# Kernel optimization log

Hardware: AMD Instinct MI355X
Metric: run time of the kernel (lower is better)

Reference implementation:

```python
import jax, jax.numpy as jnp
import numpy as np
from jax import lax

B, S, H, NH, E, L, V = 8, 512, 512, 8, 8, 6, 32000
DH = H // NH
FF = 4 * H
EPS_LN = 1e-5
EPS_GATE = 1e-8


def setup_inputs() -> dict:
    key = jax.random.key(0)
    ks = jax.random.split(key, 20)
    s = 0.02
    f = jnp.float32
    return {
        'input_ids': jax.random.randint(ks[0], (B, S), 0, V),
        'emb': (jax.random.normal(ks[1], (V, H)) * s).astype(f),
        'pos_emb': (jax.random.normal(ks[2], (S, H)) * s).astype(f),
        'attn_in_w': (jax.random.normal(ks[3], (L, 3 * H, H)) * s).astype(f),
        'attn_in_b': jnp.zeros((L, 3 * H), f),
        'attn_out_w': (jax.random.normal(ks[4], (L, H, H)) * s).astype(f),
        'attn_out_b': jnp.zeros((L, H), f),
        'ln1_g': jnp.ones((L, H), f),
        'ln1_b': jnp.zeros((L, H), f),
        'gate_w': (jax.random.normal(ks[5], (L, E, H)) * s).astype(f),
        'w1': (jax.random.normal(ks[6], (L, E, FF, H)) * s).astype(f),
        'b1': jnp.zeros((L, E, FF), f),
        'w2': (jax.random.normal(ks[7], (L, E, H, FF)) * s).astype(f),
        'b2': jnp.zeros((L, E, H), f),
        'ln2_g': jnp.ones((L, H), f),
        'ln2_b': jnp.zeros((L, H), f),
        'lnf_g': jnp.ones((H,), f),
        'lnf_b': jnp.zeros((H,), f),
        'lm_w': (jax.random.normal(ks[8], (V, H)) * s).astype(f),
    }


def _ln(x, g, b):
    m = jnp.mean(x, axis=-1, keepdims=True)
    v = jnp.mean(jnp.square(x - m), axis=-1, keepdims=True)
    return (x - m) * lax.rsqrt(v + EPS_LN) * g + b


def _forward(input_ids, emb, pos_emb, attn_in_w, attn_in_b, attn_out_w, attn_out_b,
             ln1_g, ln1_b, gate_w, w1, b1, w2, b2, ln2_g, ln2_b, lnf_g, lnf_b, lm_w):
    b_, s_ = input_ids.shape
    x = emb[input_ids] + pos_emb[jnp.arange(s_)][None]  # [B,S,H]

    def layer(x, p):
        in_w, in_b, out_w, out_b, l1g, l1b, gw, W1, B1, W2, B2, l2g, l2b = p
        # --- multi-head self attention (torch nn.MultiheadAttention math) ---
        qkv = x @ in_w.T + in_b                       # [B,S,3H]
        q, k, v = jnp.split(qkv, 3, axis=-1)
        q = q.reshape(b_, s_, NH, DH)
        k = k.reshape(b_, s_, NH, DH)
        v = v.reshape(b_, s_, NH, DH)
        scores = jnp.einsum('bqhd,bkhd->bhqk', q, k) / jnp.sqrt(jnp.float32(DH))
        att = jax.nn.softmax(scores, axis=-1)
        o = jnp.einsum('bhqk,bkhd->bqhd', att, v).reshape(b_, s_, H)
        o = o @ out_w.T + out_b
        x = _ln(x + o, l1g, l1b)
        # --- MoE MLP (top-1 switch routing) ---
        xf = x.reshape(-1, H)                          # [T,H]
        gate_scores = jax.nn.softmax(xf @ gw.T, axis=-1)  # [T,E]
        idx = jnp.argmax(gate_scores, axis=-1)         # [T]
        top = jnp.max(gate_scores, axis=-1)            # [T]
        gate = top / (top + EPS_GATE)                  # top-1 normalization
        hid = jax.nn.relu(jnp.einsum('th,efh->tef', xf, W1) + B1)  # [T,E,FF]
        ye = jnp.einsum('tef,ehf->teh', hid, W2) + B2               # [T,E,H]
        comb = jax.nn.one_hot(idx, E, dtype=xf.dtype) * gate[:, None]
        moe = jnp.einsum('te,teh->th', comb, ye)
        x = _ln(x + moe.reshape(b_, s_, H), l2g, l2b)
        # load balancing loss
        rp = gate_scores.mean(axis=0)
        eu = jax.nn.one_hot(idx, E, dtype=xf.dtype).mean(axis=0)
        lb = jnp.float32(E) * jnp.sum(rp * eu)
        return x, lb

    x, lbs = lax.scan(layer, x, (attn_in_w, attn_in_b, attn_out_w, attn_out_b,
                                 ln1_g, ln1_b, gate_w, w1, b1, w2, b2, ln2_g, ln2_b))
    logits = _ln(x, lnf_g, lnf_b) @ lm_w.T
    return logits, jnp.mean(lbs)


def reference(input_ids, emb, pos_emb, attn_in_w, attn_in_b, attn_out_w, attn_out_b,
              ln1_g, ln1_b, gate_w, w1, b1, w2, b2, ln2_g, ln2_b, lnf_g, lnf_b, lm_w):
    return _forward(input_ids, emb, pos_emb, attn_in_w, attn_in_b, attn_out_w, attn_out_b,
                    ln1_g, ln1_b, gate_w, w1, b1, w2, b2, ln2_g, ln2_b, lnf_g, lnf_b, lm_w)
```

## Files before the change

kernel.cpp:

```cpp
#include <hip/hip_runtime.h>
#include <math.h>


constexpr int CB = 8;
constexpr int CS = 512;
constexpr int CH = 512;
constexpr int CNH = 8;
constexpr int CDH = 64;
constexpr int CE = 8;
constexpr int CFF = 2048;
constexpr int CL = 6;
constexpr int CV = 32000;
constexpr int CT = CB * CS;
constexpr int CH3 = 3 * CH;

__global__ __launch_bounds__(64) void k_init(int* cnt, float* lbacc) {
  int tid = threadIdx.x;
  if (tid < CE) cnt[tid] = 0;
  if (tid == 0) *lbacc = 0.f;
}

__global__ __launch_bounds__(256) void k_embed(const int* __restrict__ ids,
                                               const float* __restrict__ emb,
                                               const float* __restrict__ pos,
                                               float* __restrict__ x) {
  int i = blockIdx.x * 256 + threadIdx.x;
  int t = i / (CH / 4);
  int h4 = i % (CH / 4);
  int id = ids[t];
  float4 e = ((const float4*)(emb + (size_t)id * CH))[h4];
  float4 p = ((const float4*)(pos + (size_t)(t % CS) * CH))[h4];
  float4 r;
  r.x = e.x + p.x; r.y = e.y + p.y; r.z = e.z + p.z; r.w = e.w + p.w;
  ((float4*)(x + (size_t)t * CH))[h4] = r;
}

__global__ __launch_bounds__(256) void k_gemm_bt(const float* __restrict__ A,
                                                 const float* __restrict__ W,
                                                 const float* __restrict__ bias,
                                                 float* __restrict__ C,
                                                 int N, int K) {
  __shared__ __align__(16) float As[16][64];
  __shared__ __align__(16) float Ws[16][64];
  int tid = threadIdx.x;
  int m0 = blockIdx.y * 64, n0 = blockIdx.x * 64;
  int lr = tid >> 2, lk = (tid & 3) << 2;
  int tx = tid & 15, ty = tid >> 4;
  float acc[4][4] = {};
  for (int k0 = 0; k0 < K; k0 += 16) {
    float4 a = *(const float4*)(A + (size_t)(m0 + lr) * K + k0 + lk);
    float4 w = *(const float4*)(W + (size_t)(n0 + lr) * K + k0 + lk);
    As[lk + 0][lr] = a.x; As[lk + 1][lr] = a.y; As[lk + 2][lr] = a.z; As[lk + 3][lr] = a.w;
    Ws[lk + 0][lr] = w.x; Ws[lk + 1][lr] = w.y; Ws[lk + 2][lr] = w.z; Ws[lk + 3][lr] = w.w;
    __syncthreads();
#pragma unroll
    for (int kk = 0; kk < 16; ++kk) {
      float ar[4], wr[4];
#pragma unroll
      for (int i = 0; i < 4; i++) ar[i] = As[kk][ty * 4 + i];
#pragma unroll
      for (int j = 0; j < 4; j++) wr[j] = Ws[kk][tx * 4 + j];
#pragma unroll
      for (int i = 0; i < 4; i++)
#pragma unroll
        for (int j = 0; j < 4; j++) acc[i][j] += ar[i] * wr[j];
    }
    __syncthreads();
  }
  float4 bv = make_float4(0.f, 0.f, 0.f, 0.f);
  if (bias) bv = *(const float4*)(bias + n0 + tx * 4);
#pragma unroll
  for (int i = 0; i < 4; i++) {
    float4 r;
    r.x = acc[i][0] + bv.x; r.y = acc[i][1] + bv.y;
    r.z = acc[i][2] + bv.z; r.w = acc[i][3] + bv.w;
    *(float4*)(C + (size_t)(m0 + ty * 4 + i) * N + n0 + tx * 4) = r;
  }
}

__global__ __launch_bounds__(256) void k_gemm_qk(const float* __restrict__ qkv,
                                                 float* __restrict__ sc) {
  int bh = blockIdx.z, b = bh >> 3, hd = bh & 7;
  const float* Qb = qkv + (size_t)b * CS * CH3 + hd * CDH;
  const float* Kb = Qb + CH;
  __shared__ __align__(16) float As[16][64];
  __shared__ __align__(16) float Bs[16][64];
  int tid = threadIdx.x;
  int m0 = blockIdx.y * 64, n0 = blockIdx.x * 64;
  int lr = tid >> 2, lk = (tid & 3) << 2;
  int tx = tid & 15, ty = tid >> 4;
  float acc[4][4] = {};
  for (int k0 = 0; k0 < CDH; k0 += 16) {
    float4 a = *(const float4*)(Qb + (size_t)(m0 + lr) * CH3 + k0 + lk);
    float4 w = *(const float4*)(Kb + (size_t)(n0 + lr) * CH3 + k0 + lk);
    As[lk + 0][lr] = a.x; As[lk + 1][lr] = a.y; As[lk + 2][lr] = a.z; As[lk + 3][lr] = a.w;
    Bs[lk + 0][lr] = w.x; Bs[lk + 1][lr] = w.y; Bs[lk + 2][lr] = w.z; Bs[lk + 3][lr] = w.w;
    __syncthreads();
#pragma unroll
    for (int kk = 0; kk < 16; ++kk) {
      float ar[4], wr[4];
#pragma unroll
      for (int i = 0; i < 4; i++) ar[i] = As[kk][ty * 4 + i];
#pragma unroll
      for (int j = 0; j < 4; j++) wr[j] = Bs[kk][tx * 4 + j];
#pragma unroll
      for (int i = 0; i < 4; i++)
#pragma unroll
        for (int j = 0; j < 4; j++) acc[i][j] += ar[i] * wr[j];
    }
    __syncthreads();
  }
#pragma unroll
  for (int i = 0; i < 4; i++) {
    float4 r;
    r.x = acc[i][0] * 0.125f; r.y = acc[i][1] * 0.125f;
    r.z = acc[i][2] * 0.125f; r.w = acc[i][3] * 0.125f;
    *(float4*)(sc + ((size_t)bh * CS + m0 + ty * 4 + i) * CS + n0 + tx * 4) = r;
  }
}

__global__ __launch_bounds__(256) void k_softmax(float* __restrict__ sc) {
  size_t row = blockIdx.x;
  float* r = sc + row * CS;
  int tid = threadIdx.x;
  float v0 = r[tid], v1 = r[tid + 256];
  __shared__ float red[4];
  __shared__ float bval;
  int lane = tid & 63, wid = tid >> 6;
  float m = fmaxf(v0, v1);
#pragma unroll
  for (int o = 32; o; o >>= 1) m = fmaxf(m, __shfl_down(m, o, 64));
  if (!lane) red[wid] = m;
  __syncthreads();
  if (!tid) bval = fmaxf(fmaxf(red[0], red[1]), fmaxf(red[2], red[3]));
  __syncthreads();
  float mx = bval;
  float e0 = expf(v0 - mx), e1 = expf(v1 - mx);
  float s = e0 + e1;
#pragma unroll
  for (int o = 32; o; o >>= 1) s += __shfl_down(s, o, 64);
  __syncthreads();
  if (!lane) red[wid] = s;
  __syncthreads();
  if (!tid) bval = red[0] + red[1] + red[2] + red[3];
  __syncthreads();
  float sum = bval;
  r[tid] = e0 / sum;
  r[tid + 256] = e1 / sum;
}

__global__ __launch_bounds__(256) void k_gemm_pv(const float* __restrict__ sc,
                                                 const float* __restrict__ qkv,
                                                 float* __restrict__ o) {
  int bh = blockIdx.z, b = bh >> 3, hd = bh & 7;
  const float* A = sc + (size_t)bh * CS * CS;
  const float* Vb = qkv + (size_t)b * CS * CH3 + 2 * CH + hd * CDH;
  __shared__ __align__(16) float As[16][64];
  __shared__ __align__(16) float Bs[16][64];
  int tid = threadIdx.x;
  int m0 = blockIdx.y * 64;
  int lr = tid >> 2, lk = (tid & 3) << 2;
  int jr = tid >> 4, dc = (tid & 15) << 2;
  int tx = tid & 15, ty = tid >> 4;
  float acc[4][4] = {};
  for (int k0 = 0; k0 < CS; k0 += 16) {
    float4 a = *(const float4*)(A + (size_t)(m0 + lr) * CS + k0 + lk);
    As[lk + 0][lr] = a.x; As[lk + 1][lr] = a.y; As[lk + 2][lr] = a.z; As[lk + 3][lr] = a.w;
    float4 v = *(const float4*)(Vb + (size_t)(k0 + jr) * CH3 + dc);
    *(float4*)&Bs[jr][dc] = v;
    __syncthreads();
#pragma unroll
    for (int kk = 0; kk < 16; ++kk) {
      float ar[4], br[4];
#pragma unroll
      for (int i = 0; i < 4; i++) ar[i] = As[kk][ty * 4 + i];
#pragma unroll
      for (int j = 0; j < 4; j++) br[j] = Bs[kk][tx * 4 + j];
#pragma unroll
      for (int i = 0; i < 4; i++)
#pragma unroll
        for (int j = 0; j < 4; j++) acc[i][j] += ar[i] * br[j];
    }
    __syncthreads();
  }
#pragma unroll
  for (int i = 0; i < 4; i++) {
    float4 r;
    r.x = acc[i][0]; r.y = acc[i][1]; r.z = acc[i][2]; r.w = acc[i][3];
    *(float4*)(o + ((size_t)b * CS + m0 + ty * 4 + i) * CH + hd * CDH + tx * 4) = r;
  }
}

__global__ __launch_bounds__(256) void k_add_ln(const float* __restrict__ xin,
                                                const float* __restrict__ resid,
                                                const float* __restrict__ g,
                                                const float* __restrict__ b,
                                                float* __restrict__ xout) {
  int t = blockIdx.x, tid = threadIdx.x;
  float v0 = xin[(size_t)t * CH + tid];
  float v1 = xin[(size_t)t * CH + tid + 256];
  if (resid) {
    v0 += resid[(size_t)t * CH + tid];
    v1 += resid[(size_t)t * CH + tid + 256];
  }
  __shared__ float red[4];
  __shared__ float stat;
  int lane = tid & 63, wid = tid >> 6;
  float s = v0 + v1;
#pragma unroll
  for (int o = 32; o; o >>= 1) s += __shfl_down(s, o, 64);
  if (!lane) red[wid] = s;
  __syncthreads();
  if (!tid) stat = (red[0] + red[1] + red[2] + red[3]) * (1.f / CH);
  __syncthreads();
  float m = stat;
  float d0 = v0 - m, d1 = v1 - m;
  float q = d0 * d0 + d1 * d1;
#pragma unroll
  for (int o = 32; o; o >>= 1) q += __shfl_down(q, o, 64);
  __syncthreads();
  if (!lane) red[wid] = q;
  __syncthreads();
  if (!tid) stat = rsqrtf((red[0] + red[1] + red[2] + red[3]) * (1.f / CH) + 1e-5f);
  __syncthreads();
  float rs = stat;
  xout[(size_t)t * CH + tid] = d0 * rs * g[tid] + b[tid];
  xout[(size_t)t * CH + tid + 256] = d1 * rs * g[tid + 256] + b[tid + 256];
}

__global__ __launch_bounds__(256) void k_gate(const float* __restrict__ xf,
                                              const float* __restrict__ gw,
                                              float* __restrict__ probs,
                                              float* __restrict__ gate,
                                              int* __restrict__ cnt,
                                              int* __restrict__ toklist) {
  int t = blockIdx.x, tid = threadIdx.x;
  float part[CE];
#pragma unroll
  for (int e = 0; e < CE; e++) part[e] = 0.f;
  for (int h = tid; h < CH; h += 256) {
    float xv = xf[(size_t)t * CH + h];
#pragma unroll
    for (int e = 0; e < CE; e++) part[e] += xv * gw[e * CH + h];
  }
  __shared__ float red[CE][4];
  int lane = tid & 63, wid = tid >> 6;
#pragma unroll
  for (int e = 0; e < CE; e++) {
    float v = part[e];
#pragma unroll
    for (int o = 32; o; o >>= 1) v += __shfl_down(v, o, 64);
    if (!lane) red[e][wid] = v;
  }
  __syncthreads();
  if (tid == 0) {
    float lg[CE], mx = -1e30f;
#pragma unroll
    for (int e = 0; e < CE; e++) {
      lg[e] = red[e][0] + red[e][1] + red[e][2] + red[e][3];
      mx = fmaxf(mx, lg[e]);
    }
    float p[CE], sum = 0.f;
#pragma unroll
    for (int e = 0; e < CE; e++) { p[e] = expf(lg[e] - mx); sum += p[e]; }
    float best = -1.f; int bi = 0;
#pragma unroll
    for (int e = 0; e < CE; e++) {
      p[e] /= sum;
      probs[(size_t)t * CE + e] = p[e];
      if (p[e] > best) { best = p[e]; bi = e; }
    }
    gate[t] = best / (best + 1e-8f);
    int pos = atomicAdd(&cnt[bi], 1);
    toklist[bi * CT + pos] = t;
  }
}

__global__ __launch_bounds__(256) void k_moe1(const float* __restrict__ xf,
                                              const float* __restrict__ w1,
                                              const float* __restrict__ b1,
                                              const int* __restrict__ cnt,
                                              const int* __restrict__ toklist,
                                              float* __restrict__ hid, int l) {
  int e = blockIdx.z;
  int n = cnt[e];
  int r0 = blockIdx.y * 64;
  if (r0 >= n) return;
  __shared__ int toks[64];
  int tid = threadIdx.x;
  if (tid < 64) toks[tid] = (r0 + tid < n) ? toklist[e * CT + r0 + tid] : -1;
  __syncthreads();
  const float* W = w1 + (size_t)(l * CE + e) * CFF * CH;
  const float* bb = b1 + (size_t)(l * CE + e) * CFF;
  int f0 = blockIdx.x * 64;
  __shared__ __align__(16) float As[16][64];
  __shared__ __align__(16) float Ws[16][64];
  int lr = tid >> 2, lk = (tid & 3) << 2;
  int tx = tid & 15, ty = tid >> 4;
  int tokA = toks[lr];
  float acc[4][4] = {};
  for (int k0 = 0; k0 < CH; k0 += 16) {
    float4 a = make_float4(0.f, 0.f, 0.f, 0.f);
    if (tokA >= 0) a = *(const float4*)(xf + (size_t)tokA * CH + k0 + lk);
    float4 w = *(const float4*)(W + (size_t)(f0 + lr) * CH + k0 + lk);
    As[lk + 0][lr] = a.x; As[lk + 1][lr] = a.y; As[lk + 2][lr] = a.z; As[lk + 3][lr] = a.w;
    Ws[lk + 0][lr] = w.x; Ws[lk + 1][lr] = w.y; Ws[lk + 2][lr] = w.z; Ws[lk + 3][lr] = w.w;
    __syncthreads();
#pragma unroll
    for (int kk = 0; kk < 16; ++kk) {
      float ar[4], wr[4];
#pragma unroll
      for (int i = 0; i < 4; i++) ar[i] = As[kk][ty * 4 + i];
#pragma unroll
      for (int j = 0; j < 4; j++) wr[j] = Ws[kk][tx * 4 + j];
#pragma unroll
      for (int i = 0; i < 4; i++)
#pragma unroll
        for (int j = 0; j < 4; j++) acc[i][j] += ar[i] * wr[j];
    }
    __syncthreads();
  }
  float4 bv = *(const float4*)(bb + f0 + tx * 4);
#pragma unroll
  for (int i = 0; i < 4; i++) {
    int tok = toks[ty * 4 + i];
    if (tok < 0) continue;
    float4 r;
    r.x = fmaxf(acc[i][0] + bv.x, 0.f);
    r.y = fmaxf(acc[i][1] + bv.y, 0.f);
    r.z = fmaxf(acc[i][2] + bv.z, 0.f);
    r.w = fmaxf(acc[i][3] + bv.w, 0.f);
    *(float4*)(hid + (size_t)tok * CFF + f0 + tx * 4) = r;
  }
}

__global__ __launch_bounds__(256) void k_moe2(const float* __restrict__ hid,
                                              const float* __restrict__ w2,
                                              const float* __restrict__ b2,
                                              const int* __restrict__ cnt,
                                              const int* __restrict__ toklist,
                                              const float* __restrict__ gate,
                                              float* __restrict__ moe, int l) {
  int e = blockIdx.z;
  int n = cnt[e];
  int r0 = blockIdx.y * 64;
  if (r0 >= n) return;
  __shared__ int toks[64];
  int tid = threadIdx.x;
  if (tid < 64) toks[tid] = (r0 + tid < n) ? toklist[e * CT + r0 + tid] : -1;
  __syncthreads();
  const float* W = w2 + (size_t)(l * CE + e) * CH * CFF;
  const float* bb = b2 + (size_t)(l * CE + e) * CH;
  int h0 = blockIdx.x * 64;
  __shared__ __align__(16) float As[16][64];
  __shared__ __align__(16) float Ws[16][64];
  int lr = tid >> 2, lk = (tid & 3) << 2;
  int tx = tid & 15, ty = tid >> 4;
  int tokA = toks[lr];
  float acc[4][4] = {};
  for (int k0 = 0; k0 < CFF; k0 += 16) {
    float4 a = make_float4(0.f, 0.f, 0.f, 0.f);
    if (tokA >= 0) a = *(const float4*)(hid + (size_t)tokA * CFF + k0 + lk);
    float4 w = *(const float4*)(W + (size_t)(h0 + lr) * CFF + k0 + lk);
    As[lk + 0][lr] = a.x; As[lk + 1][lr] = a.y; As[lk + 2][lr] = a.z; As[lk + 3][lr] = a.w;
    Ws[lk + 0][lr] = w.x; Ws[lk + 1][lr] = w.y; Ws[lk + 2][lr] = w.z; Ws[lk + 3][lr] = w.w;
    __syncthreads();
#pragma unroll
    for (int kk = 0; kk < 16; ++kk) {
      float ar[4], wr[4];
#pragma unroll
      for (int i = 0; i < 4; i++) ar[i] = As[kk][ty * 4 + i];
#pragma unroll
      for (int j = 0; j < 4; j++) wr[j] = Ws[kk][tx * 4 + j];
#pragma unroll
      for (int i = 0; i < 4; i++)
#pragma unroll
        for (int j = 0; j < 4; j++) acc[i][j] += ar[i] * wr[j];
    }
    __syncthreads();
  }
  float4 bv = *(const float4*)(bb + h0 + tx * 4);
#pragma unroll
  for (int i = 0; i < 4; i++) {
    int tok = toks[ty * 4 + i];
    if (tok < 0) continue;
    float gv = gate[tok];
    float4 r;
    r.x = gv * (acc[i][0] + bv.x);
    r.y = gv * (acc[i][1] + bv.y);
    r.z = gv * (acc[i][2] + bv.z);
    r.w = gv * (acc[i][3] + bv.w);
    *(float4*)(moe + (size_t)tok * CH + h0 + tx * 4) = r;
  }
}

__global__ __launch_bounds__(256) void k_lb(const float* __restrict__ probs,
                                            int* __restrict__ cnt,
                                            float* __restrict__ lbacc) {
  int tid = threadIdx.x;
  float part[CE];
#pragma unroll
  for (int e = 0; e < CE; e++) part[e] = 0.f;
  for (int t = tid; t < CT; t += 256) {
#pragma unroll
    for (int e = 0; e < CE; e++) part[e] += probs[(size_t)t * CE + e];
  }
  __shared__ float red[CE][4];
  int lane = tid & 63, wid = tid >> 6;
#pragma unroll
  for (int e = 0; e < CE; e++) {
    float v = part[e];
#pragma unroll
    for (int o = 32; o; o >>= 1) v += __shfl_down(v, o, 64);
    if (!lane) red[e][wid] = v;
  }
  __syncthreads();
  if (tid == 0) {
    float lb = 0.f;
#pragma unroll
    for (int e = 0; e < CE; e++) {
      float rp = (red[e][0] + red[e][1] + red[e][2] + red[e][3]) / (float)CT;
      float eu = (float)cnt[e] / (float)CT;
      lb += rp * eu;
    }
    lbacc[0] += (float)CE * lb;
  }
  __syncthreads();
  if (tid < CE) cnt[tid] = 0;
}

__global__ void k_write_lb(const float* __restrict__ lbacc, float* __restrict__ out) {
  out[(size_t)CT * CV] = lbacc[0] / (float)CL;
}

extern "C" void kernel_launch(void* const* d_in, const int* in_sizes, int n_in,
                              void* d_out, int out_size, void* d_ws, size_t ws_size,
                              hipStream_t stream) {
  const int* ids = (const int*)d_in[0];
  const float* emb = (const float*)d_in[1];
  const float* pos = (const float*)d_in[2];
  const float* aiw = (const float*)d_in[3];
  const float* aib = (const float*)d_in[4];
  const float* aow = (const float*)d_in[5];
  const float* aob = (const float*)d_in[6];
  const float* l1g = (const float*)d_in[7];
  const float* l1b = (const float*)d_in[8];
  const float* gw = (const float*)d_in[9];
  const float* w1 = (const float*)d_in[10];
  const float* b1 = (const float*)d_in[11];
  const float* w2 = (const float*)d_in[12];
  const float* b2 = (const float*)d_in[13];
  const float* l2g = (const float*)d_in[14];
  const float* l2b = (const float*)d_in[15];
  const float* lnfg = (const float*)d_in[16];
  const float* lnfb = (const float*)d_in[17];
  const float* lmw = (const float*)d_in[18];
  float* out = (float*)d_out;

  float* ws = (float*)d_ws;
  size_t off = 0;
  float* x = ws + off;      off += (size_t)CT * CH;
  float* qkv = ws + off;    off += (size_t)CT * CH3;
  float* sc = ws + off;     off += (size_t)CB * CNH * CS * CS;
  float* attno = ws + off;  off += (size_t)CT * CH;
  float* hid = ws + off;    off += (size_t)CT * CFF;
  float* moe = ws + off;    off += (size_t)CT * CH;
  float* probs = ws + off;  off += (size_t)CT * CE;
  float* gate = ws + off;   off += (size_t)CT;
  float* lbacc = ws + off;  off += 1;
  int* cnt = (int*)(ws + off);
  int* toklist = cnt + CE;

  dim3 blk(256);
  k_init<<<1, 64, 0, stream>>>(cnt, lbacc);
  k_embed<<<(CT * CH / 4) / 256, blk, 0, stream>>>(ids, emb, pos, x);
  for (int l = 0; l < CL; l++) {
    k_gemm_bt<<<dim3(CH3 / 64, CT / 64), blk, 0, stream>>>(
        x, aiw + (size_t)l * CH3 * CH, aib + (size_t)l * CH3, qkv, CH3, CH);
    k_gemm_qk<<<dim3(CS / 64, CS / 64, CB * CNH), blk, 0, stream>>>(qkv, sc);
    k_softmax<<<CB * CNH * CS, blk, 0, stream>>>(sc);
    k_gemm_pv<<<dim3(1, CS / 64, CB * CNH), blk, 0, stream>>>(sc, qkv, attno);
    k_gemm_bt<<<dim3(CH / 64, CT / 64), blk, 0, stream>>>(
        attno, aow + (size_t)l * CH * CH, aob + (size_t)l * CH, moe, CH, CH);
    k_add_ln<<<CT, blk, 0, stream>>>(x, moe, l1g + (size_t)l * CH, l1b + (size_t)l * CH, x);
    k_gate<<<CT, blk, 0, stream>>>(x, gw + (size_t)l * CE * CH, probs, gate, cnt, toklist);
    k_moe1<<<dim3(CFF / 64, CT / 64, CE), blk, 0, stream>>>(x, w1, b1, cnt, toklist, hid, l);
    k_moe2<<<dim3(CH / 64, CT / 64, CE), blk, 0, stream>>>(hid, w2, b2, cnt, toklist, gate, moe, l);
    k_add_ln<<<CT, blk, 0, stream>>>(x, moe, l2g + (size_t)l * CH, l2b + (size_t)l * CH, x);
    k_lb<<<1, blk, 0, stream>>>(probs, cnt, lbacc);
  }
  k_add_ln<<<CT, blk, 0, stream>>>(x, nullptr, lnfg, lnfb, attno);
  k_gemm_bt<<<dim3(CV / 64, CT / 64), blk, 0, stream>>>(attno, lmw, nullptr, out, CV, CH);
  k_write_lb<<<1, 1, 0, stream>>>(lbacc, out);
}
```

Baseline: 7.454 ms.

## Use bf16 MFMA for final MoE layer and LM head, enlarge fp32 GEMM tiles

Replaces the 64x64 fp32 GEMMs with a shared 128x128 tile core that gives each thread an 8x8 register block, used for QKV, QK scores, the output projection and the MoE layers. For the last layer's MoE and the vocabulary projection, weights are converted to bf16 and multiplied with MFMA 16x16x32 bf16 instructions, and the LayerNorm kernels also write bf16 copies of activations. The load-balance reduction is restructured with a transposed probs layout. The bf16 path only on the last layer and the LM head lowers precision and adds weight conversion passes on every call.

```diff
diff --git a/kernel.cpp b/kernel.cpp
--- a/kernel.cpp
+++ b/kernel.cpp
@@ -2,17 +2,22 @@
 #include <math.h>
 
 
-constexpr int CB = 8;
-constexpr int CS = 512;
-constexpr int CH = 512;
-constexpr int CNH = 8;
-constexpr int CDH = 64;
-constexpr int CE = 8;
-constexpr int CFF = 2048;
-constexpr int CL = 6;
-constexpr int CV = 32000;
-constexpr int CT = CB * CS;
-constexpr int CH3 = 3 * CH;
+typedef unsigned short u16;
+typedef __attribute__((ext_vector_type(8))) short s8v;
+typedef __attribute__((ext_vector_type(4))) float f4v;
+
+constexpr int CB = 8, CS = 512, CH = 512, CNH = 8, CDH = 64, CE = 8;
+constexpr int CFF = 2048, CL = 6, CV = 32000;
+constexpr int CT = CB * CS, CH3 = 3 * CH;
+
+__device__ __forceinline__ u16 f2b(float f) {
+  unsigned u = __builtin_bit_cast(unsigned, f);
+  return (u16)((u + 0x7fffu + ((u >> 16) & 1u)) >> 16);
+}
+__device__ __forceinline__ float b2f(u16 h) {
+  unsigned u = ((unsigned)h) << 16;
+  return __builtin_bit_cast(float, u);
+}
 
 __global__ __launch_bounds__(64) void k_init(int* cnt, float* lbacc) {
   int tid = threadIdx.x;
@@ -23,7 +28,8 @@
 __global__ __launch_bounds__(256) void k_embed(const int* __restrict__ ids,
                                                const float* __restrict__ emb,
                                                const float* __restrict__ pos,
-                                               float* __restrict__ x) {
+                                               float* __restrict__ x,
+                                               u16* __restrict__ xbf) {
   int i = blockIdx.x * 256 + threadIdx.x;
   int t = i / (CH / 4);
   int h4 = i % (CH / 4);
@@ -33,90 +39,253 @@
   float4 r;
   r.x = e.x + p.x; r.y = e.y + p.y; r.z = e.z + p.z; r.w = e.w + p.w;
   ((float4*)(x + (size_t)t * CH))[h4] = r;
-}
-
-__global__ __launch_bounds__(256) void k_gemm_bt(const float* __restrict__ A,
-                                                 const float* __restrict__ W,
-                                                 const float* __restrict__ bias,
-                                                 float* __restrict__ C,
-                                                 int N, int K) {
-  __shared__ __align__(16) float As[16][64];
-  __shared__ __align__(16) float Ws[16][64];
-  int tid = threadIdx.x;
-  int m0 = blockIdx.y * 64, n0 = blockIdx.x * 64;
-  int lr = tid >> 2, lk = (tid & 3) << 2;
-  int tx = tid & 15, ty = tid >> 4;
-  float acc[4][4] = {};
+  unsigned long long pk = (unsigned long long)f2b(r.x) |
+                          ((unsigned long long)f2b(r.y) << 16) |
+                          ((unsigned long long)f2b(r.z) << 32) |
+                          ((unsigned long long)f2b(r.w) << 48);
+  *(unsigned long long*)(xbf + (size_t)t * CH + h4 * 4) = pk;
+}
+
+template <bool GATHER, int EP>
+__device__ __forceinline__ void mm32_core(
+    const float* __restrict__ A, int lda, const float* __restrict__ W, int ldw,
+    int K, const float* __restrict__ bias, float scale,
+    float* __restrict__ C, int ldc, int m0, int n0,
+    const int* __restrict__ tokl, int nrows, const float* __restrict__ gatev) {
+  __shared__ __align__(16) float As[16][128];
+  __shared__ __align__(16) float Ws[16][128];
+  __shared__ int toks[128];
+  const int tid = threadIdx.x;
+  if (GATHER) {
+    if (tid < 128) toks[tid] = (tid < nrows) ? tokl[tid] : -1;
+    __syncthreads();
+  }
+  const int lr = tid >> 1, half = tid & 1;
+  const float* gA;
+  if (GATHER) {
+    int t = toks[lr]; if (t < 0) t = 0;
+    gA = A + (size_t)t * lda + half * 8;
+  } else {
+    gA = A + (size_t)(m0 + lr) * lda + half * 8;
+  }
+  const float* gW = W + (size_t)(n0 + lr) * ldw + half * 8;
+  const int tx = tid & 15, ty = tid >> 4;
+  float acc[8][8];
+#pragma unroll
+  for (int i = 0; i < 8; i++)
+#pragma unroll
+    for (int j = 0; j < 8; j++) acc[i][j] = 0.f;
+
   for (int k0 = 0; k0 < K; k0 += 16) {
-    float4 a = *(const float4*)(A + (size_t)(m0 + lr) * K + k0 + lk);
-    float4 w = *(const float4*)(W + (size_t)(n0 + lr) * K + k0 + lk);
-    As[lk + 0][lr] = a.x; As[lk + 1][lr] = a.y; As[lk + 2][lr] = a.z; As[lk + 3][lr] = a.w;
-    Ws[lk + 0][lr] = w.x; Ws[lk + 1][lr] = w.y; Ws[lk + 2][lr] = w.z; Ws[lk + 3][lr] = w.w;
+    float4 a0 = *(const float4*)(gA + k0);
+    float4 a1 = *(const float4*)(gA + k0 + 4);
+    float4 w0 = *(const float4*)(gW + k0);
+    float4 w1 = *(const float4*)(gW + k0 + 4);
+    __syncthreads();
+    int kb = half * 8;
+    As[kb + 0][lr] = a0.x; As[kb + 1][lr] = a0.y; As[kb + 2][lr] = a0.z; As[kb + 3][lr] = a0.w;
+    As[kb + 4][lr] = a1.x; As[kb + 5][lr] = a1.y; As[kb + 6][lr] = a1.z; As[kb + 7][lr] = a1.w;
+    Ws[kb + 0][lr] = w0.x; Ws[kb + 1][lr] = w0.y; Ws[kb + 2][lr] = w0.z; Ws[kb + 3][lr] = w0.w;
+    Ws[kb + 4][lr] = w1.x; Ws[kb + 5][lr] = w1.y; Ws[kb + 6][lr] = w1.z; Ws[kb + 7][lr] = w1.w;
     __syncthreads();
 #pragma unroll
     for (int kk = 0; kk < 16; ++kk) {
-      float ar[4], wr[4];
-#pragma unroll
-      for (int i = 0; i < 4; i++) ar[i] = As[kk][ty * 4 + i];
-#pragma unroll
-      for (int j = 0; j < 4; j++) wr[j] = Ws[kk][tx * 4 + j];
-#pragma unroll
-      for (int i = 0; i < 4; i++)
-#pragma unroll
-        for (int j = 0; j < 4; j++) acc[i][j] += ar[i] * wr[j];
-    }
-    __syncthreads();
-  }
-  float4 bv = make_float4(0.f, 0.f, 0.f, 0.f);
-  if (bias) bv = *(const float4*)(bias + n0 + tx * 4);
-#pragma unroll
-  for (int i = 0; i < 4; i++) {
-    float4 r;
-    r.x = acc[i][0] + bv.x; r.y = acc[i][1] + bv.y;
-    r.z = acc[i][2] + bv.z; r.w = acc[i][3] + bv.w;
-    *(float4*)(C + (size_t)(m0 + ty * 4 + i) * N + n0 + tx * 4) = r;
-  }
-}
-
-__global__ __launch_bounds__(256) void k_gemm_qk(const float* __restrict__ qkv,
-                                                 float* __restrict__ sc) {
-  int bh = blockIdx.z, b = bh >> 3, hd = bh & 7;
-  const float* Qb = qkv + (size_t)b * CS * CH3 + hd * CDH;
-  const float* Kb = Qb + CH;
-  __shared__ __align__(16) float As[16][64];
-  __shared__ __align__(16) float Bs[16][64];
-  int tid = threadIdx.x;
-  int m0 = blockIdx.y * 64, n0 = blockIdx.x * 64;
-  int lr = tid >> 2, lk = (tid & 3) << 2;
-  int tx = tid & 15, ty = tid >> 4;
-  float acc[4][4] = {};
-  for (int k0 = 0; k0 < CDH; k0 += 16) {
-    float4 a = *(const float4*)(Qb + (size_t)(m0 + lr) * CH3 + k0 + lk);
-    float4 w = *(const float4*)(Kb + (size_t)(n0 + lr) * CH3 + k0 + lk);
-    As[lk + 0][lr] = a.x; As[lk + 1][lr] = a.y; As[lk + 2][lr] = a.z; As[lk + 3][lr] = a.w;
-    Bs[lk + 0][lr] = w.x; Bs[lk + 1][lr] = w.y; Bs[lk + 2][lr] = w.z; Bs[lk + 3][lr] = w.w;
-    __syncthreads();
-#pragma unroll
-    for (int kk = 0; kk < 16; ++kk) {
-      float ar[4], wr[4];
-#pragma unroll
-      for (int i = 0; i < 4; i++) ar[i] = As[kk][ty * 4 + i];
-#pragma unroll
-      for (int j = 0; j < 4; j++) wr[j] = Bs[kk][tx * 4 + j];
-#pragma unroll
-      for (int i = 0; i < 4; i++)
-#pragma unroll
-        for (int j = 0; j < 4; j++) acc[i][j] += ar[i] * wr[j];
-    }
-    __syncthreads();
-  }
-#pragma unroll
-  for (int i = 0; i < 4; i++) {
-    float4 r;
-    r.x = acc[i][0] * 0.125f; r.y = acc[i][1] * 0.125f;
-    r.z = acc[i][2] * 0.125f; r.w = acc[i][3] * 0.125f;
-    *(float4*)(sc + ((size_t)bh * CS + m0 + ty * 4 + i) * CS + n0 + tx * 4) = r;
-  }
+      float ar[8], br[8];
+      *(float4*)(ar + 0) = *(const float4*)&As[kk][ty * 4];
+      *(float4*)(ar + 4) = *(const float4*)&As[kk][64 + ty * 4];
+      *(float4*)(br + 0) = *(const float4*)&Ws[kk][tx * 4];
+      *(float4*)(br + 4) = *(const float4*)&Ws[kk][64 + tx * 4];
+#pragma unroll
+      for (int i = 0; i < 8; i++)
+#pragma unroll
+        for (int j = 0; j < 8; j++) acc[i][j] = fmaf(ar[i], br[j], acc[i][j]);
+    }
+  }
+#pragma unroll
+  for (int gj = 0; gj < 2; gj++) {
+    int cloc = gj * 64 + tx * 4;
+    float4 bv = make_float4(0.f, 0.f, 0.f, 0.f);
+    if (EP != 1 && bias) bv = *(const float4*)(bias + n0 + cloc);
+#pragma unroll
+    for (int gi = 0; gi < 2; gi++) {
+#pragma unroll
+      for (int i = 0; i < 4; i++) {
+        int rloc = gi * 64 + ty * 4 + i;
+        float4 v;
+        v.x = acc[gi * 4 + i][gj * 4 + 0];
+        v.y = acc[gi * 4 + i][gj * 4 + 1];
+        v.z = acc[gi * 4 + i][gj * 4 + 2];
+        v.w = acc[gi * 4 + i][gj * 4 + 3];
+        if (EP == 0) {
+          v.x += bv.x; v.y += bv.y; v.z += bv.z; v.w += bv.w;
+          *(float4*)(C + (size_t)(m0 + rloc) * ldc + n0 + cloc) = v;
+        } else if (EP == 1) {
+          v.x *= scale; v.y *= scale; v.z *= scale; v.w *= scale;
+          *(float4*)(C + (size_t)(m0 + rloc) * ldc + n0 + cloc) = v;
+        } else if (EP == 3) {
+          int tok = toks[rloc];
+          if (tok >= 0) {
+            v.x = fmaxf(v.x + bv.x, 0.f); v.y = fmaxf(v.y + bv.y, 0.f);
+            v.z = fmaxf(v.z + bv.z, 0.f); v.w = fmaxf(v.w + bv.w, 0.f);
+            *(float4*)(C + (size_t)tok * ldc + n0 + cloc) = v;
+          }
+        } else {
+          int tok = toks[rloc];
+          if (tok >= 0) {
+            float gv = gatev[tok];
+            v.x = (v.x + bv.x) * gv; v.y = (v.y + bv.y) * gv;
+            v.z = (v.z + bv.z) * gv; v.w = (v.w + bv.w) * gv;
+            *(float4*)(C + (size_t)tok * ldc + n0 + cloc) = v;
+          }
+        }
+      }
+    }
+  }
+}
+
+__global__ __launch_bounds__(256) void k_lin32(const float* A, int lda, const float* W, int ldw,
+                                               int K, const float* bias, float* C, int ldc) {
+  mm32_core<false, 0>(A, lda, W, ldw, K, bias, 1.f, C, ldc,
+                      blockIdx.y * 128, blockIdx.x * 128, nullptr, 0, nullptr);
+}
+__global__ __launch_bounds__(256) void k_qk32(const float* qkv, float* sc) {
+  int z = blockIdx.z;
+  const float* A = qkv + (size_t)(z >> 3) * CS * CH3 + (z & 7) * CDH;
+  mm32_core<false, 1>(A, CH3, A + CH, CH3, CDH, nullptr, 0.125f,
+                      sc + (size_t)z * CS * CS, CS,
+                      blockIdx.y * 128, blockIdx.x * 128, nullptr, 0, nullptr);
+}
+__global__ __launch_bounds__(256) void k_moe1_32(const float* x, const float* w1, const float* b1,
+                                                 const int* cnt, const int* tokl, float* hid) {
+  int e = blockIdx.z, n = cnt[e], r0 = blockIdx.y * 128;
+  if (r0 >= n) return;
+  mm32_core<true, 3>(x, CH, w1 + (size_t)e * CFF * CH, CH, CH, b1 + e * CFF, 1.f,
+                     hid, CFF, 0, blockIdx.x * 128, tokl + e * CT + r0, n - r0, nullptr);
+}
+__global__ __launch_bounds__(256) void k_moe2_32(const float* hid, const float* w2, const float* b2,
+                                                 const int* cnt, const int* tokl,
+                                                 const float* gate, float* outp) {
+  int e = blockIdx.z, n = cnt[e], r0 = blockIdx.y * 128;
+  if (r0 >= n) return;
+  mm32_core<true, 4>(hid, CFF, w2 + (size_t)e * CH * CFF, CFF, CFF, b2 + e * CH, 1.f,
+                     outp, CH, 0, blockIdx.x * 128, tokl + e * CT + r0, n - r0, gate);
+}
+
+template <bool GATHER, int EP>
+__device__ __forceinline__ void mmbf_core(
+    const u16* __restrict__ A, int lda, const u16* __restrict__ W, int ldw,
+    int K, const float* __restrict__ bias,
+    float* __restrict__ Cf, u16* __restrict__ Cb, int ldc, int m0, int n0,
+    const int* __restrict__ tokl, int nrows, const float* __restrict__ gatev) {
+  __shared__ __align__(16) u16 As[128 * 40];
+  __shared__ __align__(16) u16 Ws[128 * 40];
+  __shared__ int toks[128];
+  const int tid = threadIdx.x, lane = tid & 63, w = tid >> 6;
+  const int wr = w >> 1, wc = w & 1, r = lane & 15, g = lane >> 4;
+  if (GATHER) {
+    if (tid < 128) toks[tid] = (tid < nrows) ? tokl[tid] : -1;
+    __syncthreads();
+  }
+  const int sr = tid >> 1, sh = (tid & 1) * 16;
+  const u16* gA;
+  if (GATHER) {
+    int t = toks[sr]; if (t < 0) t = 0;
+    gA = A + (size_t)t * lda + sh;
+  } else {
+    gA = A + (size_t)(m0 + sr) * lda + sh;
+  }
+  const u16* gW = W + (size_t)(n0 + sr) * ldw + sh;
+  u16* lA = As + sr * 40 + sh;
+  u16* lW = Ws + sr * 40 + sh;
+  f4v acc[4][4];
+#pragma unroll
+  for (int m = 0; m < 4; m++)
+#pragma unroll
+    for (int n = 0; n < 4; n++) { f4v z = {0.f, 0.f, 0.f, 0.f}; acc[m][n] = z; }
+
+  for (int k0 = 0; k0 < K; k0 += 32) {
+    s8v a0 = *(const s8v*)(gA + k0);
+    s8v a1 = *(const s8v*)(gA + k0 + 8);
+    s8v w0 = *(const s8v*)(gW + k0);
+    s8v w1 = *(const s8v*)(gW + k0 + 8);
+    __syncthreads();
+    *(s8v*)lA = a0; *(s8v*)(lA + 8) = a1;
+    *(s8v*)lW = w0; *(s8v*)(lW + 8) = w1;
+    __syncthreads();
+    s8v av[4], bv[4];
+#pragma unroll
+    for (int m = 0; m < 4; m++)
+      av[m] = *(const s8v*)(As + (wr * 64 + m * 16 + r) * 40 + g * 8);
+#pragma unroll
+    for (int n = 0; n < 4; n++)
+      bv[n] = *(const s8v*)(Ws + (wc * 64 + n * 16 + r) * 40 + g * 8);
+#pragma unroll
+    for (int m = 0; m < 4; m++)
+#pragma unroll
+      for (int n = 0; n < 4; n++)
+        acc[m][n] = __builtin_amdgcn_mfma_f32_16x16x32_bf16(av[m], bv[n], acc[m][n], 0, 0, 0);
+  }
+  const int cb = n0 + wc * 64;
+#pragma unroll
+  for (int m = 0; m < 4; m++) {
+    int wrow = wr * 64 + m * 16 + (lane >> 4) * 4;
+#pragma unroll
+    for (int n = 0; n < 4; n++) {
+      int col = cb + n * 16 + r;
+      float bv_ = bias ? bias[col] : 0.f;
+      if (EP == 0) {
+#pragma unroll
+        for (int j = 0; j < 4; j++)
+          Cf[(size_t)(m0 + wrow + j) * ldc + col] = acc[m][n][j] + bv_;
+      } else if (EP == 3) {
+#pragma unroll
+        for (int j = 0; j < 4; j++) {
+          int tok = toks[wrow + j];
+          if (tok < 0) continue;
+          Cb[(size_t)tok * ldc + col] = f2b(fmaxf(acc[m][n][j] + bv_, 0.f));
+        }
+      } else {
+#pragma unroll
+        for (int j = 0; j < 4; j++) {
+          int tok = toks[wrow + j];
+          if (tok < 0) continue;
+          Cf[(size_t)tok * ldc + col] = (acc[m][n][j] + bv_) * gatev[tok];
+        }
+      }
+    }
+  }
+}
+
+__global__ __launch_bounds__(256) void k_linbf(const u16* A, int lda, const u16* W, int ldw,
+                                               int K, const float* bias, float* C, int ldc) {
+  mmbf_core<false, 0>(A, lda, W, ldw, K, bias, C, nullptr, ldc,
+                      blockIdx.y * 128, blockIdx.x * 128, nullptr, 0, nullptr);
+}
+__global__ __launch_bounds__(256) void k_moe1_bf(const u16* xbf, const u16* w1b, const float* b1,
+                                                 const int* cnt, const int* tokl, u16* hidb) {
+  int e = blockIdx.z, n = cnt[e], r0 = blockIdx.y * 128;
+  if (r0 >= n) return;
+  mmbf_core<true, 3>(xbf, CH, w1b + (size_t)e * CFF * CH, CH, CH, b1 + e * CFF,
+                     nullptr, hidb, CFF, 0, blockIdx.x * 128, tokl + e * CT + r0, n - r0, nullptr);
+}
+__global__ __launch_bounds__(256) void k_moe2_bf(const u16* hidb, const u16* w2b, const float* b2,
+                                                 const int* cnt, const int* tokl,
+                                                 const float* gate, float* outp) {
+  int e = blockIdx.z, n = cnt[e], r0 = blockIdx.y * 128;
+  if (r0 >= n) return;
+  mmbf_core<true, 4>(hidb, CFF, w2b + (size_t)e * CH * CFF, CFF, CFF, b2 + e * CH,
+                     outp, nullptr, CH, 0, blockIdx.x * 128, tokl + e * CT + r0, n - r0, gate);
+}
+
+__global__ __launch_bounds__(256) void k_f2b(const float* __restrict__ s, u16* __restrict__ d, int n4) {
+  int i = blockIdx.x * 256 + threadIdx.x;
+  if (i >= n4) return;
+  float4 v = ((const float4*)s)[i];
+  unsigned long long pk = (unsigned long long)f2b(v.x) |
+                          ((unsigned long long)f2b(v.y) << 16) |
+                          ((unsigned long long)f2b(v.z) << 32) |
+                          ((unsigned long long)f2b(v.w) << 48);
+  *(unsigned long long*)(d + (size_t)i * 4) = pk;
 }
 
 __global__ __launch_bounds__(256) void k_softmax(float* __restrict__ sc) {
@@ -179,7 +348,7 @@
 #pragma unroll
       for (int i = 0; i < 4; i++)
 #pragma unroll
-        for (int j = 0; j < 4; j++) acc[i][j] += ar[i] * br[j];
+        for (int j = 0; j < 4; j++) acc[i][j] = fmaf(ar[i], br[j], acc[i][j]);
     }
     __syncthreads();
   }
@@ -195,7 +364,8 @@
                                                 const float* __restrict__ resid,
                                                 const float* __restrict__ g,
                                                 const float* __restrict__ b,
-                                                float* __restrict__ xout) {
+                                                float* __restrict__ xout,
+                                                u16* __restrict__ xbf) {
   int t = blockIdx.x, tid = threadIdx.x;
   float v0 = xin[(size_t)t * CH + tid];
   float v1 = xin[(size_t)t * CH + tid + 256];
@@ -224,8 +394,12 @@
   if (!tid) stat = rsqrtf((red[0] + red[1] + red[2] + red[3]) * (1.f / CH) + 1e-5f);
   __syncthreads();
   float rs = stat;
-  xout[(size_t)t * CH + tid] = d0 * rs * g[tid] + b[tid];
-  xout[(size_t)t * CH + tid + 256] = d1 * rs * g[tid + 256] + b[tid + 256];
+  float o0 = d0 * rs * g[tid] + b[tid];
+  float o1 = d1 * rs * g[tid + 256] + b[tid + 256];
+  xout[(size_t)t * CH + tid] = o0;
+  xout[(size_t)t * CH + tid + 256] = o1;
+  xbf[(size_t)t * CH + tid] = f2b(o0);
+  xbf[(size_t)t * CH + tid + 256] = f2b(o1);
 }
 
 __global__ __launch_bounds__(256) void k_gate(const float* __restrict__ xf,
@@ -267,7 +441,7 @@
 #pragma unroll
     for (int e = 0; e < CE; e++) {
       p[e] /= sum;
-      probs[(size_t)t * CE + e] = p[e];
+      probs[(size_t)e * CT + t] = p[e];
       if (p[e] > best) { best = p[e]; bi = e; }
     }
     gate[t] = best / (best + 1e-8f);
@@ -276,157 +450,32 @@
   }
 }
 
-__global__ __launch_bounds__(256) void k_moe1(const float* __restrict__ xf,
-                                              const float* __restrict__ w1,
-                                              const float* __restrict__ b1,
-                                              const int* __restrict__ cnt,
-                                              const int* __restrict__ toklist,
-                                              float* __restrict__ hid, int l) {
-  int e = blockIdx.z;
-  int n = cnt[e];
-  int r0 = blockIdx.y * 64;
-  if (r0 >= n) return;
-  __shared__ int toks[64];
+__global__ __launch_bounds__(1024) void k_lb(const float* __restrict__ probs,
+                                             int* __restrict__ cnt,
+                                             float* __restrict__ lbacc) {
   int tid = threadIdx.x;
-  if (tid < 64) toks[tid] = (r0 + tid < n) ? toklist[e * CT + r0 + tid] : -1;
-  __syncthreads();
-  const float* W = w1 + (size_t)(l * CE + e) * CFF * CH;
-  const float* bb = b1 + (size_t)(l * CE + e) * CFF;
-  int f0 = blockIdx.x * 64;
-  __shared__ __align__(16) float As[16][64];
-  __shared__ __align__(16) float Ws[16][64];
-  int lr = tid >> 2, lk = (tid & 3) << 2;
-  int tx = tid & 15, ty = tid >> 4;
-  int tokA = toks[lr];
-  float acc[4][4] = {};
-  for (int k0 = 0; k0 < CH; k0 += 16) {
-    float4 a = make_float4(0.f, 0.f, 0.f, 0.f);
-    if (tokA >= 0) a = *(const float4*)(xf + (size_t)tokA * CH + k0 + lk);
-    float4 w = *(const float4*)(W + (size_t)(f0 + lr) * CH + k0 + lk);
-    As[lk + 0][lr] = a.x; As[lk + 1][lr] = a.y; As[lk + 2][lr] = a.z; As[lk + 3][lr] = a.w;
-    Ws[lk + 0][lr] = w.x; Ws[lk + 1][lr] = w.y; Ws[lk + 2][lr] = w.z; Ws[lk + 3][lr] = w.w;
-    __syncthreads();
-#pragma unroll
-    for (int kk = 0; kk < 16; ++kk) {
-      float ar[4], wr[4];
-#pragma unroll
-      for (int i = 0; i < 4; i++) ar[i] = As[kk][ty * 4 + i];
-#pragma unroll
-      for (int j = 0; j < 4; j++) wr[j] = Ws[kk][tx * 4 + j];
-#pragma unroll
-      for (int i = 0; i < 4; i++)
-#pragma unroll
-        for (int j = 0; j < 4; j++) acc[i][j] += ar[i] * wr[j];
-    }
-    __syncthreads();
-  }
-  float4 bv = *(const float4*)(bb + f0 + tx * 4);
-#pragma unroll
-  for (int i = 0; i < 4; i++) {
-    int tok = toks[ty * 4 + i];
-    if (tok < 0) continue;
-    float4 r;
-    r.x = fmaxf(acc[i][0] + bv.x, 0.f);
-    r.y = fmaxf(acc[i][1] + bv.y, 0.f);
-    r.z = fmaxf(acc[i][2] + bv.z, 0.f);
-    r.w = fmaxf(acc[i][3] + bv.w, 0.f);
-    *(float4*)(hid + (size_t)tok * CFF + f0 + tx * 4) = r;
-  }
-}
-
-__global__ __launch_bounds__(256) void k_moe2(const float* __restrict__ hid,
-                                              const float* __restrict__ w2,
-                                              const float* __restrict__ b2,
-                                              const int* __restrict__ cnt,
-                                              const int* __restrict__ toklist,
-                                              const float* __restrict__ gate,
-                                              float* __restrict__ moe, int l) {
-  int e = blockIdx.z;
-  int n = cnt[e];
-  int r0 = blockIdx.y * 64;
-  if (r0 >= n) return;
-  __shared__ int toks[64];
-  int tid = threadIdx.x;
-  if (tid < 64) toks[tid] = (r0 + tid < n) ? toklist[e * CT + r0 + tid] : -1;
-  __syncthreads();
-  const float* W = w2 + (size_t)(l * CE + e) * CH * CFF;
-  const float* bb = b2 + (size_t)(l * CE + e) * CH;
-  int h0 = blockIdx.x * 64;
-  __shared__ __align__(16) float As[16][64];
-  __shared__ __align__(16) float Ws[16][64];
-  int lr = tid >> 2, lk = (tid & 3) << 2;
-  int tx = tid & 15, ty = tid >> 4;
-  int tokA = toks[lr];
-  float acc[4][4] = {};
-  for (int k0 = 0; k0 < CFF; k0 += 16) {
-    float4 a = make_float4(0.f, 0.f, 0.f, 0.f);
-    if (tokA >= 0) a = *(const float4*)(hid + (size_t)tokA * CFF + k0 + lk);
-    float4 w = *(const float4*)(W + (size_t)(h0 + lr) * CFF + k0 + lk);
-    As[lk + 0][lr] = a.x; As[lk + 1][lr] = a.y; As[lk + 2][lr] = a.z; As[lk + 3][lr] = a.w;
-    Ws[lk + 0][lr] = w.x; Ws[lk + 1][lr] = w.y; Ws[lk + 2][lr] = w.z; Ws[lk + 3][lr] = w.w;
-    __syncthreads();
-#pragma unroll
-    for (int kk = 0; kk < 16; ++kk) {
-      float ar[4], wr[4];
-#pragma unroll
-      for (int i = 0; i < 4; i++) ar[i] = As[kk][ty * 4 + i];
-#pragma unroll
-      for (int j = 0; j < 4; j++) wr[j] = Ws[kk][tx * 4 + j];
-#pragma unroll
-      for (int i = 0; i < 4; i++)
-#pragma unroll
-        for (int j = 0; j < 4; j++) acc[i][j] += ar[i] * wr[j];
-    }
-    __syncthreads();
-  }
-  float4 bv = *(const float4*)(bb + h0 + tx * 4);
-#pragma unroll
-  for (int i = 0; i < 4; i++) {
-    int tok = toks[ty * 4 + i];
-    if (tok < 0) continue;
-    float gv = gate[tok];
-    float4 r;
-    r.x = gv * (acc[i][0] + bv.x);
-    r.y = gv * (acc[i][1] + bv.y);
-    r.z = gv * (acc[i][2] + bv.z);
-    r.w = gv * (acc[i][3] + bv.w);
-    *(float4*)(moe + (size_t)tok * CH + h0 + tx * 4) = r;
-  }
-}
-
-__global__ __launch_bounds__(256) void k_lb(const float* __restrict__ probs,
-                                            int* __restrict__ cnt,
-                                            float* __restrict__ lbacc) {
-  int tid = threadIdx.x;
-  float part[CE];
-#pragma unroll
-  for (int e = 0; e < CE; e++) part[e] = 0.f;
-  for (int t = tid; t < CT; t += 256) {
-#pragma unroll
-    for (int e = 0; e < CE; e++) part[e] += probs[(size_t)t * CE + e];
-  }
-  __shared__ float red[CE][4];
-  int lane = tid & 63, wid = tid >> 6;
-#pragma unroll
-  for (int e = 0; e < CE; e++) {
-    float v = part[e];
-#pragma unroll
-    for (int o = 32; o; o >>= 1) v += __shfl_down(v, o, 64);
-    if (!lane) red[e][wid] = v;
+  int e = tid >> 7, sub = tid & 127;
+  float s = 0.f;
+  for (int i = sub; i < CT; i += 128) s += probs[(size_t)e * CT + i];
+#pragma unroll
+  for (int o = 32; o; o >>= 1) s += __shfl_down(s, o, 64);
+  __shared__ float red[16];
+  __shared__ float pe[CE];
+  if ((tid & 63) == 0) red[tid >> 6] = s;
+  __syncthreads();
+  if (tid < CE) {
+    float rp = (red[tid * 2] + red[tid * 2 + 1]) * (1.f / CT);
+    float eu = (float)cnt[tid] * (1.f / CT);
+    pe[tid] = rp * eu;
+    cnt[tid] = 0;
   }
   __syncthreads();
   if (tid == 0) {
     float lb = 0.f;
 #pragma unroll
-    for (int e = 0; e < CE; e++) {
-      float rp = (red[e][0] + red[e][1] + red[e][2] + red[e][3]) / (float)CT;
-      float eu = (float)cnt[e] / (float)CT;
-      lb += rp * eu;
-    }
+    for (int e2 = 0; e2 < CE; e2++) lb += pe[e2];
     lbacc[0] += (float)CE * lb;
   }
-  __syncthreads();
-  if (tid < CE) cnt[tid] = 0;
 }
 
 __global__ void k_write_lb(const float* __restrict__ lbacc, float* __restrict__ out) {
@@ -457,39 +506,60 @@
   const float* lmw = (const float*)d_in[18];
   float* out = (float*)d_out;
 
-  float* ws = (float*)d_ws;
+  char* ws = (char*)d_ws;
   size_t off = 0;
-  float* x = ws + off;      off += (size_t)CT * CH;
-  float* qkv = ws + off;    off += (size_t)CT * CH3;
-  float* sc = ws + off;     off += (size_t)CB * CNH * CS * CS;
-  float* attno = ws + off;  off += (size_t)CT * CH;
-  float* hid = ws + off;    off += (size_t)CT * CFF;
-  float* moe = ws + off;    off += (size_t)CT * CH;
-  float* probs = ws + off;  off += (size_t)CT * CE;
-  float* gate = ws + off;   off += (size_t)CT;
-  float* lbacc = ws + off;  off += 1;
-  int* cnt = (int*)(ws + off);
-  int* toklist = cnt + CE;
+  auto alloc = [&](size_t bytes) { char* p = ws + off; off += (bytes + 255) & ~(size_t)255; return p; };
+  float* x     = (float*)alloc((size_t)CT * CH * 4);
+  u16*   x_bf  = (u16*)  alloc((size_t)CT * CH * 2);
+  u16*   xf_bf = (u16*)  alloc((size_t)CT * CH * 2);
+  float* qkv   = (float*)alloc((size_t)CT * CH3 * 4);
+  float* sc    = (float*)alloc((size_t)CB * CNH * CS * CS * 4);
+  float* attno = (float*)alloc((size_t)CT * CH * 4);
+  float* tmp   = (float*)alloc((size_t)CT * CH * 4);
+  float* hid   = (float*)alloc((size_t)CT * CFF * 4);
+  float* probs = (float*)alloc((size_t)CE * CT * 4);
+  float* gate  = (float*)alloc((size_t)CT * 4);
+  float* lbacc = (float*)alloc(256);
+  int*   cnt   = (int*)  alloc(CE * 4);
+  int*   tokl  = (int*)  alloc((size_t)CE * CT * 4);
+  u16* hid_bf = (u16*)hid;
+  u16* wbuf1  = (u16*)sc;
+  u16* wbuf2  = wbuf1 + (size_t)CE * CFF * CH;
+  u16* lmw_bf = wbuf2 + (size_t)CE * CFF * CH;
 
   dim3 blk(256);
   k_init<<<1, 64, 0, stream>>>(cnt, lbacc);
-  k_embed<<<(CT * CH / 4) / 256, blk, 0, stream>>>(ids, emb, pos, x);
+  k_embed<<<(CT * CH / 4) / 256, blk, 0, stream>>>(ids, emb, pos, x, x_bf);
   for (int l = 0; l < CL; l++) {
-    k_gemm_bt<<<dim3(CH3 / 64, CT / 64), blk, 0, stream>>>(
-        x, aiw + (size_t)l * CH3 * CH, aib + (size_t)l * CH3, qkv, CH3, CH);
-    k_gemm_qk<<<dim3(CS / 64, CS / 64, CB * CNH), blk, 0, stream>>>(qkv, sc);
+    k_lin32<<<dim3(CH3 / 128, CT / 128), blk, 0, stream>>>(
+        x, CH, aiw + (size_t)l * CH3 * CH, CH, CH, aib + (size_t)l * CH3, qkv, CH3);
+    k_qk32<<<dim3(4, 4, CB * CNH), blk, 0, stream>>>(qkv, sc);
     k_softmax<<<CB * CNH * CS, blk, 0, stream>>>(sc);
     k_gemm_pv<<<dim3(1, CS / 64, CB * CNH), blk, 0, stream>>>(sc, qkv, attno);
-    k_gemm_bt<<<dim3(CH / 64, CT / 64), blk, 0, stream>>>(
-        attno, aow + (size_t)l * CH * CH, aob + (size_t)l * CH, moe, CH, CH);
-    k_add_ln<<<CT, blk, 0, stream>>>(x, moe, l1g + (size_t)l * CH, l1b + (size_t)l * CH, x);
-    k_gate<<<CT, blk, 0, stream>>>(x, gw + (size_t)l * CE * CH, probs, gate, cnt, toklist);
-    k_moe1<<<dim3(CFF / 64, CT / 64, CE), blk, 0, stream>>>(x, w1, b1, cnt, toklist, hid, l);
-    k_moe2<<<dim3(CH / 64, CT / 64, CE), blk, 0, stream>>>(hid, w2, b2, cnt, toklist, gate, moe, l);
-    k_add_ln<<<CT, blk, 0, stream>>>(x, moe, l2g + (size_t)l * CH, l2b + (size_t)l * CH, x);
-    k_lb<<<1, blk, 0, stream>>>(probs, cnt, lbacc);
-  }
-  k_add_ln<<<CT, blk, 0, stream>>>(x, nullptr, lnfg, lnfb, attno);
-  k_gemm_bt<<<dim3(CV / 64, CT / 64), blk, 0, stream>>>(attno, lmw, nullptr, out, CV, CH);
+    k_lin32<<<dim3(CH / 128, CT / 128), blk, 0, stream>>>(
+        attno, CH, aow + (size_t)l * CH * CH, CH, CH, aob + (size_t)l * CH, tmp, CH);
+    k_add_ln<<<CT, blk, 0, stream>>>(x, tmp, l1g + (size_t)l * CH, l1b + (size_t)l * CH, x, x_bf);
+    k_gate<<<CT, blk, 0, stream>>>(x, gw + (size_t)l * CE * CH, probs, gate, cnt, tokl);
+    if (l < CL - 1) {
+      k_moe1_32<<<dim3(CFF / 128, CT / 128, CE), blk, 0, stream>>>(
+          x, w1 + (size_t)l * CE * CFF * CH, b1 + (size_t)l * CE * CFF, cnt, tokl, hid);
+      k_moe2_32<<<dim3(CH / 128, CT / 128, CE), blk, 0, stream>>>(
+          hid, w2 + (size_t)l * CE * CH * CFF, b2 + (size_t)l * CE * CH, cnt, tokl, gate, tmp);
+    } else {
+      int n4a = CE * CFF * CH / 4;
+      k_f2b<<<(n4a + 255) / 256, blk, 0, stream>>>(w1 + (size_t)l * CE * CFF * CH, wbuf1, n4a);
+      k_f2b<<<(n4a + 255) / 256, blk, 0, stream>>>(w2 + (size_t)l * CE * CH * CFF, wbuf2, n4a);
+      int n4l = CV * CH / 4;
+      k_f2b<<<(n4l + 255) / 256, blk, 0, stream>>>(lmw, lmw_bf, n4l);
+      k_moe1_bf<<<dim3(CFF / 128, CT / 128, CE), blk, 0, stream>>>(
+          x_bf, wbuf1, b1 + (size_t)l * CE * CFF, cnt, tokl, hid_bf);
+      k_moe2_bf<<<dim3(CH / 128, CT / 128, CE), blk, 0, stream>>>(
+          hid_bf, wbuf2, b2 + (size_t)l * CE * CH, cnt, tokl, gate, tmp);
+    }
+    k_add_ln<<<CT, blk, 0, stream>>>(x, tmp, l2g + (size_t)l * CH, l2b + (size_t)l * CH, x, x_bf);
+    k_lb<<<1, 1024, 0, stream>>>(probs, cnt, lbacc);
+  }
+  k_add_ln<<<CT, blk, 0, stream>>>(x, nullptr, lnfg, lnfb, tmp, xf_bf);
+  k_linbf<<<dim3(CV / 128, CT / 128), blk, 0, stream>>>(xf_bf, CH, lmw_bf, CH, CH, nullptr, out, CV);
   k_write_lb<<<1, 1, 0, stream>>>(lbacc, out);
 }
```

After: 7.190 ms. 3.5% less time.
